# Kernel tuning notes

Measured on AMD Instinct MI355X. Metric: run time of the kernel, lower is better.

The kernel has to match this reference:

```python
import jax, jax.numpy as jnp
import numpy as np

N_NODES = 100000
N_EDGES = 3200000
N_FEAT = 300
HIDDEN = 32
N_CLASSES = 10


def setup_inputs() -> dict:
    key = jax.random.key(0)
    k1, k2, k3, k4 = jax.random.split(key, 4)
    x = jax.random.normal(k1, (N_NODES, N_FEAT), dtype=jnp.float32)
    edge_index = jax.random.randint(k2, (2, N_EDGES), 0, N_NODES, dtype=jnp.int64)
    # Glorot-ish init for weights
    W1 = jax.random.normal(k3, (N_FEAT, HIDDEN), dtype=jnp.float32) * (1.0 / np.sqrt(N_FEAT))
    b1 = jnp.zeros((HIDDEN,), dtype=jnp.float32)
    W2 = jax.random.normal(k4, (HIDDEN, N_CLASSES), dtype=jnp.float32) * (1.0 / np.sqrt(HIDDEN))
    b2 = jnp.zeros((N_CLASSES,), dtype=jnp.float32)
    return {"x": x, "edge_index": edge_index, "W1": W1, "b1": b1, "W2": W2, "b2": b2}


def reference(x, edge_index, W1, b1, W2, b2):
    N = x.shape[0]
    # GCNConv default: add self-loops, symmetric normalization deg^-1/2 A deg^-1/2
    loops = jnp.arange(N, dtype=edge_index.dtype)
    src = jnp.concatenate([edge_index[0], loops])  # message sources
    dst = jnp.concatenate([edge_index[1], loops])  # aggregation targets

    deg = jax.ops.segment_sum(jnp.ones(dst.shape, dtype=x.dtype), dst, num_segments=N)
    dinv = jnp.where(deg > 0, jax.lax.rsqrt(deg), 0.0)
    norm = dinv[src] * dinv[dst]  # [E+N]

    def gcn_conv(h, W, b):
        h = h @ W                                   # [N, out] dense GEMM first (linear-then-propagate)
        msg = h[src] * norm[:, None]                # gather + scale
        out = jax.ops.segment_sum(msg, dst, num_segments=N)  # scatter-add aggregate
        return out + b

    h = jnp.tanh(gcn_conv(x, W1, b1))
    # dropout p=0.5 is identity in eval mode (training=False)
    logits = gcn_conv(h, W2, b2)
    return jax.nn.log_softmax(logits, axis=1)
```

## Files before the change

### kernel.cpp

```cpp
#include <hip/hip_runtime.h>
#include <math.h>
#include <float.h>

#define NFEAT 300
#define HID 32
#define NCLS 10
#define GP 16
#define BSZ 128
#define TILE 8192

__global__ void k_zero_i(int* __restrict__ p, int n) {
    int i = blockIdx.x * 256 + threadIdx.x;
    if (i < n) p[i] = 0;
}

__global__ __launch_bounds__(256) void k_bhist(const int* __restrict__ ei, int E, int NB,
                                               int* __restrict__ bcnt) {
    __shared__ int h[1024];
    for (int i = threadIdx.x; i < NB; i += 256) h[i] = 0;
    __syncthreads();
    for (long long i = (long long)blockIdx.x * 256 + threadIdx.x; i < E;
         i += (long long)gridDim.x * 256)
        atomicAdd(&h[ei[E + i] >> 7], 1);
    __syncthreads();
    for (int i = threadIdx.x; i < NB; i += 256) {
        int v = h[i];
        if (v) atomicAdd(&bcnt[i], v);
    }
}

__global__ void k_bscan(const int* __restrict__ bcnt, int NB, int E,
                        int* __restrict__ bases, int* __restrict__ bcur) {
    __shared__ int s[1024];
    int tid = threadIdx.x;
    int v = (tid < NB) ? bcnt[tid] : 0;
    s[tid] = v;
    __syncthreads();
    for (int off = 1; off < 1024; off <<= 1) {
        int t = (tid >= off) ? s[tid - off] : 0;
        __syncthreads();
        s[tid] += t;
        __syncthreads();
    }
    if (tid < NB) {
        int ex = s[tid] - v;
        bases[tid] = ex;
        bcur[tid] = ex;
        if (tid == NB - 1) bases[NB] = E;
    }
}

__global__ __launch_bounds__(256) void k_part(const int* __restrict__ ei, int E, int NB,
                                              int* __restrict__ bcur, int* __restrict__ pp) {
    __shared__ int hist[1024], lbase[1024], gbase[1024], lcur[1024];
    __shared__ int stage[TILE], tgt[TILE];
    int* part = gbase;
    int tid = threadIdx.x;
    long long t0 = (long long)blockIdx.x * TILE;
    int nE = (int)(((long long)E - t0 < TILE) ? ((long long)E - t0) : TILE);

    for (int b = tid; b < NB; b += 256) hist[b] = 0;
    __syncthreads();
    for (int i = tid; i < nE; i += 256) {
        int d = ei[E + t0 + i];
        atomicAdd(&hist[d >> 7], 1);
    }
    __syncthreads();
    int i0 = tid * 4;
    int c0 = (i0 + 0 < NB) ? hist[i0 + 0] : 0;
    int c1 = (i0 + 1 < NB) ? hist[i0 + 1] : 0;
    int c2 = (i0 + 2 < NB) ? hist[i0 + 2] : 0;
    int c3 = (i0 + 3 < NB) ? hist[i0 + 3] : 0;
    int sum = c0 + c1 + c2 + c3;
    part[tid] = sum;
    __syncthreads();
    for (int off = 1; off < 256; off <<= 1) {
        int t = (tid >= off) ? part[tid - off] : 0;
        __syncthreads();
        part[tid] += t;
        __syncthreads();
    }
    int ex = part[tid] - sum;
    if (i0 + 0 < NB) { lbase[i0 + 0] = ex; ex += c0; }
    if (i0 + 1 < NB) { lbase[i0 + 1] = ex; ex += c1; }
    if (i0 + 2 < NB) { lbase[i0 + 2] = ex; ex += c2; }
    if (i0 + 3 < NB) { lbase[i0 + 3] = ex; ex += c3; }
    __syncthreads();
    for (int b = tid; b < NB; b += 256) {
        int h = hist[b];
        gbase[b] = h ? atomicAdd(&bcur[b], h) : 0;
        lcur[b] = 0;
    }
    __syncthreads();
    for (int i = tid; i < nE; i += 256) {
        int s = ei[t0 + i];
        int d = ei[E + t0 + i];
        int b = d >> 7;
        int lo = atomicAdd(&lcur[b], 1);
        int slot = lbase[b] + lo;
        stage[slot] = ((d - (b << 7)) << 17) | s;
        tgt[slot] = gbase[b] + lo;
    }
    __syncthreads();
    for (int i = tid; i < nE; i += 256)
        pp[tgt[i]] = stage[i];
}

__global__ __launch_bounds__(256) void k_csr(const int* __restrict__ pp,
                                             const int* __restrict__ bases,
                                             int N, int E,
                                             int* __restrict__ rowptr,
                                             float* __restrict__ dinv,
                                             int* __restrict__ col) {
    __shared__ int lc[BSZ], rp[BSZ], sc[BSZ];
    int b = blockIdx.x, tid = threadIdx.x;
    int n0 = b << 7;
    int base = bases[b];
    int cnt = bases[b + 1] - base;
    if (tid < BSZ) lc[tid] = 0;
    __syncthreads();
    for (int i = tid; i < cnt; i += 256)
        atomicAdd(&lc[pp[base + i] >> 17], 1);
    __syncthreads();
    if (tid < BSZ) sc[tid] = lc[tid];
    __syncthreads();
    for (int off = 1; off < BSZ; off <<= 1) {
        int t = (tid < BSZ && tid >= off) ? sc[tid - off] : 0;
        __syncthreads();
        if (tid < BSZ) sc[tid] += t;
        __syncthreads();
    }
    if (tid < BSZ) {
        int node = n0 + tid;
        int ex = base + sc[tid] - lc[tid];
        rp[tid] = ex;
        if (node < N) {
            rowptr[node] = ex;
            dinv[node] = rsqrtf((float)(lc[tid] + 1));
            if (node == N - 1) rowptr[N] = E;
        }
        lc[tid] = 0;
    }
    __syncthreads();
    for (int i = tid; i < cnt; i += 256) {
        int v = pp[base + i];
        int dl = v >> 17;
        int lo = atomicAdd(&lc[dl], 1);
        col[rp[dl] + lo] = v & 0x1FFFF;
    }
}

__global__ __launch_bounds__(256) void k_gemm1(const float* __restrict__ x,
                                               const float* __restrict__ W1,
                                               const float* __restrict__ dinv,
                                               float* __restrict__ h1s, int n) {
    int lane = threadIdx.x & 63;
    int q = __builtin_amdgcn_readfirstlane(threadIdx.x >> 6);
    int node = blockIdx.x * 64 + lane;
    bool valid = node < n;
    const float4* xr = reinterpret_cast<const float4*>(
        x + (size_t)(valid ? node : (n - 1)) * NFEAT);
    const float* Wq = W1 + q * 8;
    float acc[8];
#pragma unroll
    for (int i = 0; i < 8; ++i) acc[i] = 0.f;
#pragma unroll 5
    for (int c = 0; c < NFEAT / 4; ++c) {
        float4 xv = xr[c];
        const float* w0 = Wq + (size_t)(4 * c + 0) * HID;
        const float* w1 = Wq + (size_t)(4 * c + 1) * HID;
        const float* w2 = Wq + (size_t)(4 * c + 2) * HID;
        const float* w3 = Wq + (size_t)(4 * c + 3) * HID;
#pragma unroll
        for (int i = 0; i < 8; ++i) {
            acc[i] = fmaf(xv.x, w0[i], acc[i]);
            acc[i] = fmaf(xv.y, w1[i], acc[i]);
            acc[i] = fmaf(xv.z, w2[i], acc[i]);
            acc[i] = fmaf(xv.w, w3[i], acc[i]);
        }
    }
    if (valid) {
        float dd = dinv[node];
        float4* dst = reinterpret_cast<float4*>(h1s + (size_t)node * HID + q * 8);
        dst[0] = make_float4(dd * acc[0], dd * acc[1], dd * acc[2], dd * acc[3]);
        dst[1] = make_float4(dd * acc[4], dd * acc[5], dd * acc[6], dd * acc[7]);
    }
}

__global__ __launch_bounds__(256) void k_agg1(const float* __restrict__ h1s,
                                              const int* __restrict__ rowptr,
                                              const int* __restrict__ col,
                                              const float* __restrict__ dinv,
                                              const float* __restrict__ b1,
                                              float* __restrict__ h2, int n) {
    int node = blockIdx.x * 32 + (threadIdx.x >> 3);
    int l = threadIdx.x & 7;
    if (node >= n) return;
    const float4* h4 = reinterpret_cast<const float4*>(h1s);
    int beg = rowptr[node], end = rowptr[node + 1];
    float4 a0 = h4[(size_t)node * 8 + l];
    float4 a1 = make_float4(0.f, 0.f, 0.f, 0.f);
    float4 a2 = make_float4(0.f, 0.f, 0.f, 0.f);
    float4 a3 = make_float4(0.f, 0.f, 0.f, 0.f);
    int j = beg;
    for (; j + 3 < end; j += 4) {
        int s0 = col[j], s1 = col[j + 1], s2 = col[j + 2], s3 = col[j + 3];
        float4 v0 = h4[(size_t)s0 * 8 + l];
        float4 v1 = h4[(size_t)s1 * 8 + l];
        float4 v2 = h4[(size_t)s2 * 8 + l];
        float4 v3 = h4[(size_t)s3 * 8 + l];
        a0.x += v0.x; a0.y += v0.y; a0.z += v0.z; a0.w += v0.w;
        a1.x += v1.x; a1.y += v1.y; a1.z += v1.z; a1.w += v1.w;
        a2.x += v2.x; a2.y += v2.y; a2.z += v2.z; a2.w += v2.w;
        a3.x += v3.x; a3.y += v3.y; a3.z += v3.z; a3.w += v3.w;
    }
    for (; j < end; ++j) {
        float4 v = h4[(size_t)col[j] * 8 + l];
        a0.x += v.x; a0.y += v.y; a0.z += v.z; a0.w += v.w;
    }
    float dd = dinv[node];
    const float4* b4 = reinterpret_cast<const float4*>(b1);
    float4 bv = b4[l];
    float4 r;
    r.x = tanhf(fmaf(dd, (a0.x + a1.x) + (a2.x + a3.x), bv.x));
    r.y = tanhf(fmaf(dd, (a0.y + a1.y) + (a2.y + a3.y), bv.y));
    r.z = tanhf(fmaf(dd, (a0.z + a1.z) + (a2.z + a3.z), bv.z));
    r.w = tanhf(fmaf(dd, (a0.w + a1.w) + (a2.w + a3.w), bv.w));
    reinterpret_cast<float4*>(h2)[(size_t)node * 8 + l] = r;
}

__global__ __launch_bounds__(256) void k_gemm2(const float* __restrict__ h2,
                                               const float* __restrict__ W2,
                                               const float* __restrict__ dinv,
                                               float* __restrict__ gs, int n) {
    __shared__ float Ws[HID * NCLS];
    for (int i = threadIdx.x; i < HID * NCLS; i += 256) Ws[i] = W2[i];
    __syncthreads();
    int t = blockIdx.x * 256 + threadIdx.x;
    int node = t >> 4, c = t & 15;
    if (node >= n || c >= NCLS) return;
    const float* hr = h2 + (size_t)node * HID;
    float acc = 0.f;
#pragma unroll
    for (int k = 0; k < HID; ++k) acc = fmaf(hr[k], Ws[k * NCLS + c], acc);
    gs[(size_t)node * GP + c] = acc * dinv[node];
}

__global__ __launch_bounds__(256) void k_agg2(const float* __restrict__ gs,
                                              const int* __restrict__ rowptr,
                                              const int* __restrict__ col,
                                              const float* __restrict__ dinv,
                                              const float* __restrict__ b2,
                                              float* __restrict__ out, int n) {
    int node = blockIdx.x * 64 + (threadIdx.x >> 2);
    int l = threadIdx.x & 3;
    if (node >= n) return;
    const float4* g4 = reinterpret_cast<const float4*>(gs);
    int beg = rowptr[node], end = rowptr[node + 1];
    float4 a0 = g4[(size_t)node * 4 + l];
    float4 a1 = make_float4(0.f, 0.f, 0.f, 0.f);
    int j = beg;
    for (; j + 1 < end; j += 2) {
        int s0 = col[j], s1 = col[j + 1];
        float4 v0 = g4[(size_t)s0 * 4 + l];
        float4 v1 = g4[(size_t)s1 * 4 + l];
        a0.x += v0.x; a0.y += v0.y; a0.z += v0.z; a0.w += v0.w;
        a1.x += v1.x; a1.y += v1.y; a1.z += v1.z; a1.w += v1.w;
    }
    if (j < end) {
        float4 v = g4[(size_t)col[j] * 4 + l];
        a0.x += v.x; a0.y += v.y; a0.z += v.z; a0.w += v.w;
    }
    float dd = dinv[node];
    int c0 = 4 * l;
    float val[4];
    float av[4] = {a0.x + a1.x, a0.y + a1.y, a0.z + a1.z, a0.w + a1.w};
#pragma unroll
    for (int i = 0; i < 4; ++i) {
        int c = c0 + i;
        val[i] = (c < NCLS) ? fmaf(dd, av[i], b2[c]) : -FLT_MAX;
    }
    float m = fmaxf(fmaxf(val[0], val[1]), fmaxf(val[2], val[3]));
    m = fmaxf(m, __shfl_xor(m, 1, 4));
    m = fmaxf(m, __shfl_xor(m, 2, 4));
    float s = 0.f;
#pragma unroll
    for (int i = 0; i < 4; ++i)
        if (c0 + i < NCLS) s += expf(val[i] - m);
    s += __shfl_xor(s, 1, 4);
    s += __shfl_xor(s, 2, 4);
    float ls = m + logf(s);
    float* orow = out + (size_t)node * NCLS;
#pragma unroll
    for (int i = 0; i < 4; ++i)
        if (c0 + i < NCLS) orow[c0 + i] = val[i] - ls;
}

static inline size_t align256(size_t b) { return (b + 255) & ~(size_t)255; }

extern "C" void kernel_launch(void* const* d_in, const int* in_sizes, int n_in,
                              void* d_out, int out_size, void* d_ws, size_t ws_size,
                              hipStream_t stream) {
    const float* x  = (const float*)d_in[0];
    const int*   ei = (const int*)d_in[1];
    const float* W1 = (const float*)d_in[2];
    const float* b1 = (const float*)d_in[3];
    const float* W2 = (const float*)d_in[4];
    const float* b2 = (const float*)d_in[5];
    float* out = (float*)d_out;

    const int N = in_sizes[0] / NFEAT;
    const int E = in_sizes[1] / 2;
    const int NB = (N + BSZ - 1) / BSZ;

    char* p = (char*)d_ws;
    int* bcnt   = (int*)p;  p += align256(1024 * 4);
    int* bases  = (int*)p;  p += align256(1025 * 4);
    int* bcur   = (int*)p;  p += align256(1024 * 4);
    int* rowptr = (int*)p;  p += align256((size_t)(N + 1) * 4);
    int* pp     = (int*)p;  p += align256((size_t)E * 4);
    int* col    = (int*)p;  p += align256((size_t)E * 4);
    float* dinv = (float*)p; p += align256((size_t)N * 4);
    float* h1s  = (float*)p; p += align256((size_t)N * HID * 4);
    float* h2   = (float*)p; p += align256((size_t)N * HID * 4);
    float* gs   = h1s;

    dim3 B(256);
    int nT = (E + TILE - 1) / TILE;

    k_zero_i<<<4, B, 0, stream>>>(bcnt, 1024);
    k_bhist<<<128, B, 0, stream>>>(ei, E, NB, bcnt);
    k_bscan<<<1, 1024, 0, stream>>>(bcnt, NB, E, bases, bcur);
    k_part<<<nT, B, 0, stream>>>(ei, E, NB, bcur, pp);
    k_csr<<<NB, B, 0, stream>>>(pp, bases, N, E, rowptr, dinv, col);

    k_gemm1<<<(N + 63) / 64, B, 0, stream>>>(x, W1, dinv, h1s, N);
    k_agg1<<<(N + 31) / 32, B, 0, stream>>>(h1s, rowptr, col, dinv, b1, h2, N);
    k_gemm2<<<(N * 16 + 255) / 256, B, 0, stream>>>(h2, W2, dinv, gs, N);
    k_agg2<<<(N + 63) / 64, B, 0, stream>>>(gs, rowptr, col, dinv, b2, out, N);
}
```

Before: 260.0 us.

## Stage x rows through double-buffered LDS with coalesced loads in GEMM1

The first-layer GEMM previously had each lane stream its own 1200-byte x row with strided float4 loads, giving poorly coalesced global access. The kernel now cooperatively loads 64 rows in 60-feature chunks with coalesced float4 reads into padded shared memory (stride 61 to avoid bank conflicts), double-buffered so the next chunk's global loads are issued in registers before computing the current chunk. This adds LDS usage (about 31 KB per block) and block barriers, which may reduce occupancy.

```diff
diff --git a/kernel.cpp b/kernel.cpp
--- a/kernel.cpp
+++ b/kernel.cpp
@@ -154,32 +154,63 @@
                                                const float* __restrict__ W1,
                                                const float* __restrict__ dinv,
                                                float* __restrict__ h1s, int n) {
-    int lane = threadIdx.x & 63;
-    int q = __builtin_amdgcn_readfirstlane(threadIdx.x >> 6);
-    int node = blockIdx.x * 64 + lane;
-    bool valid = node < n;
-    const float4* xr = reinterpret_cast<const float4*>(
-        x + (size_t)(valid ? node : (n - 1)) * NFEAT);
-    const float* Wq = W1 + q * 8;
+    __shared__ float xs[2][64 * 61];
+    int tid = threadIdx.x;
+    int lane = tid & 63;
+    int q = __builtin_amdgcn_readfirstlane(tid >> 6);
+    int n0 = blockIdx.x * 64;
+    int node = n0 + lane;
+    const float4* x4 = reinterpret_cast<const float4*>(x);
+
     float acc[8];
 #pragma unroll
     for (int i = 0; i < 8; ++i) acc[i] = 0.f;
-#pragma unroll 5
-    for (int c = 0; c < NFEAT / 4; ++c) {
-        float4 xv = xr[c];
-        const float* w0 = Wq + (size_t)(4 * c + 0) * HID;
-        const float* w1 = Wq + (size_t)(4 * c + 1) * HID;
-        const float* w2 = Wq + (size_t)(4 * c + 2) * HID;
-        const float* w3 = Wq + (size_t)(4 * c + 3) * HID;
-#pragma unroll
-        for (int i = 0; i < 8; ++i) {
-            acc[i] = fmaf(xv.x, w0[i], acc[i]);
-            acc[i] = fmaf(xv.y, w1[i], acc[i]);
-            acc[i] = fmaf(xv.z, w2[i], acc[i]);
-            acc[i] = fmaf(xv.w, w3[i], acc[i]);
+
+    for (int i = tid; i < 960; i += 256) {
+        int r = i / 15, f = i % 15;
+        int gr = min(n0 + r, n - 1);
+        float4 v = x4[(size_t)gr * 75 + f];
+        float* d = &xs[0][r * 61 + f * 4];
+        d[0] = v.x; d[1] = v.y; d[2] = v.z; d[3] = v.w;
+    }
+    __syncthreads();
+
+    int cur = 0;
+    for (int ch = 0; ch < 5; ++ch) {
+        float4 v0, v1, v2, v3;
+        int i0 = tid, i1 = tid + 256, i2 = tid + 512, i3 = tid + 768;
+        bool more = (ch + 1 < 5);
+        if (more) {
+            int cb = (ch + 1) * 15;
+            { int r = i0 / 15, f = i0 % 15; v0 = x4[(size_t)min(n0 + r, n - 1) * 75 + cb + f]; }
+            { int r = i1 / 15, f = i1 % 15; v1 = x4[(size_t)min(n0 + r, n - 1) * 75 + cb + f]; }
+            { int r = i2 / 15, f = i2 % 15; v2 = x4[(size_t)min(n0 + r, n - 1) * 75 + cb + f]; }
+            if (i3 < 960) { int r = i3 / 15, f = i3 % 15; v3 = x4[(size_t)min(n0 + r, n - 1) * 75 + cb + f]; }
         }
-    }
-    if (valid) {
+        const float* xrow = &xs[cur][lane * 61];
+        const float* wbase = W1 + (size_t)(ch * 60) * HID + q * 8;
+#pragma unroll 6
+        for (int j = 0; j < 60; ++j) {
+            float xv = xrow[j];
+            const float* w = wbase + (size_t)j * HID;
+#pragma unroll
+            for (int i = 0; i < 8; ++i) acc[i] = fmaf(xv, w[i], acc[i]);
+        }
+        if (more) {
+            float* xb = xs[cur ^ 1];
+            { int r = i0 / 15, f = i0 % 15; float* d = &xb[r * 61 + f * 4];
+              d[0] = v0.x; d[1] = v0.y; d[2] = v0.z; d[3] = v0.w; }
+            { int r = i1 / 15, f = i1 % 15; float* d = &xb[r * 61 + f * 4];
+              d[0] = v1.x; d[1] = v1.y; d[2] = v1.z; d[3] = v1.w; }
+            { int r = i2 / 15, f = i2 % 15; float* d = &xb[r * 61 + f * 4];
+              d[0] = v2.x; d[1] = v2.y; d[2] = v2.z; d[3] = v2.w; }
+            if (i3 < 960) { int r = i3 / 15, f = i3 % 15; float* d = &xb[r * 61 + f * 4];
+              d[0] = v3.x; d[1] = v3.y; d[2] = v3.z; d[3] = v3.w; }
+        }
+        __syncthreads();
+        cur ^= 1;
+    }
+    if (node < n) {
         float dd = dinv[node];
         float4* dst = reinterpret_cast<float4*>(h1s + (size_t)node * HID + q * 8);
         dst[0] = make_float4(dd * acc[0], dd * acc[1], dd * acc[2], dd * acc[3]);
```

Result: no change. 261.7 us (median of 5 runs) (+0.7%).

## Stage x and W1 chunks through shared memory in first GEMM

Applied to the files above, without the earlier changes.

Rewrites the x@W1 kernel to cooperatively load 128-node by 48-feature tiles of x, plus the matching W1 rows, into shared memory. Each thread then computes 16 outputs instead of 8, so the x row is read once per block rather than by four waves. The old version had each lane stream its own 1200-byte x row with strided float4 loads. The new one coalesces global reads across the block and reuses W through LDS float4 broadcasts, at the cost of block syncs and more registers.

```diff
diff --git a/kernel.cpp b/kernel.cpp
--- a/kernel.cpp
+++ b/kernel.cpp
@@ -154,36 +154,64 @@
                                                const float* __restrict__ W1,
                                                const float* __restrict__ dinv,
                                                float* __restrict__ h1s, int n) {
-    int lane = threadIdx.x & 63;
-    int q = __builtin_amdgcn_readfirstlane(threadIdx.x >> 6);
-    int node = blockIdx.x * 64 + lane;
-    bool valid = node < n;
-    const float4* xr = reinterpret_cast<const float4*>(
-        x + (size_t)(valid ? node : (n - 1)) * NFEAT);
-    const float* Wq = W1 + q * 8;
-    float acc[8];
-#pragma unroll
-    for (int i = 0; i < 8; ++i) acc[i] = 0.f;
-#pragma unroll 5
-    for (int c = 0; c < NFEAT / 4; ++c) {
-        float4 xv = xr[c];
-        const float* w0 = Wq + (size_t)(4 * c + 0) * HID;
-        const float* w1 = Wq + (size_t)(4 * c + 1) * HID;
-        const float* w2 = Wq + (size_t)(4 * c + 2) * HID;
-        const float* w3 = Wq + (size_t)(4 * c + 3) * HID;
-#pragma unroll
-        for (int i = 0; i < 8; ++i) {
-            acc[i] = fmaf(xv.x, w0[i], acc[i]);
-            acc[i] = fmaf(xv.y, w1[i], acc[i]);
-            acc[i] = fmaf(xv.z, w2[i], acc[i]);
-            acc[i] = fmaf(xv.w, w3[i], acc[i]);
+    __shared__ float xs[128 * 49];
+    __shared__ float Wc[48 * HID];
+    int tid = threadIdx.x;
+    int lane = tid & 63;
+    int w = __builtin_amdgcn_readfirstlane(tid >> 6);
+    int g = w & 1;
+    int p = w >> 1;
+    int n0 = blockIdx.x * 128;
+    int node = n0 + 64 * g + lane;
+    const float4* x4 = reinterpret_cast<const float4*>(x);
+    const float4* w4 = reinterpret_cast<const float4*>(W1);
+
+    float acc[16];
+#pragma unroll
+    for (int i = 0; i < 16; ++i) acc[i] = 0.f;
+
+    for (int ch = 0; ch < 7; ++ch) {
+        int j0 = ch * 48;
+        int CL = (NFEAT - j0 < 48) ? (NFEAT - j0) : 48;
+        int nf4 = CL >> 2;
+        __syncthreads();
+        int tot = 128 * nf4;
+        for (int i = tid; i < tot; i += 256) {
+            int r = i / nf4, f = i - r * nf4;
+            int gr = min(n0 + r, n - 1);
+            float4 v = x4[(size_t)gr * 75 + ch * 12 + f];
+            float* d = &xs[r * 49 + f * 4];
+            d[0] = v.x; d[1] = v.y; d[2] = v.z; d[3] = v.w;
         }
-    }
-    if (valid) {
+        for (int i = tid; i < CL * 8; i += 256)
+            reinterpret_cast<float4*>(Wc)[i] = w4[(size_t)j0 * 8 + i];
+        __syncthreads();
+        const float* xrow = &xs[(64 * g + lane) * 49];
+        const float4* Wq = reinterpret_cast<const float4*>(Wc) + 4 * p;
+#pragma unroll 4
+        for (int j = 0; j < CL; ++j) {
+            float xv = xrow[j];
+            float4 w0 = Wq[j * 8 + 0];
+            float4 w1 = Wq[j * 8 + 1];
+            float4 w2 = Wq[j * 8 + 2];
+            float4 w3 = Wq[j * 8 + 3];
+            acc[0]  = fmaf(xv, w0.x, acc[0]);  acc[1]  = fmaf(xv, w0.y, acc[1]);
+            acc[2]  = fmaf(xv, w0.z, acc[2]);  acc[3]  = fmaf(xv, w0.w, acc[3]);
+            acc[4]  = fmaf(xv, w1.x, acc[4]);  acc[5]  = fmaf(xv, w1.y, acc[5]);
+            acc[6]  = fmaf(xv, w1.z, acc[6]);  acc[7]  = fmaf(xv, w1.w, acc[7]);
+            acc[8]  = fmaf(xv, w2.x, acc[8]);  acc[9]  = fmaf(xv, w2.y, acc[9]);
+            acc[10] = fmaf(xv, w2.z, acc[10]); acc[11] = fmaf(xv, w2.w, acc[11]);
+            acc[12] = fmaf(xv, w3.x, acc[12]); acc[13] = fmaf(xv, w3.y, acc[13]);
+            acc[14] = fmaf(xv, w3.z, acc[14]); acc[15] = fmaf(xv, w3.w, acc[15]);
+        }
+    }
+    if (node < n) {
         float dd = dinv[node];
-        float4* dst = reinterpret_cast<float4*>(h1s + (size_t)node * HID + q * 8);
-        dst[0] = make_float4(dd * acc[0], dd * acc[1], dd * acc[2], dd * acc[3]);
-        dst[1] = make_float4(dd * acc[4], dd * acc[5], dd * acc[6], dd * acc[7]);
+        float4* dst = reinterpret_cast<float4*>(h1s + (size_t)node * HID + 16 * p);
+#pragma unroll
+        for (int qq = 0; qq < 4; ++qq)
+            dst[qq] = make_float4(dd * acc[4 * qq], dd * acc[4 * qq + 1],
+                                  dd * acc[4 * qq + 2], dd * acc[4 * qq + 3]);
     }
 }
 
@@ -334,7 +362,7 @@
     k_part<<<nT, B, 0, stream>>>(ei, E, NB, bcur, pp);
     k_csr<<<NB, B, 0, stream>>>(pp, bases, N, E, rowptr, dinv, col);
 
-    k_gemm1<<<(N + 63) / 64, B, 0, stream>>>(x, W1, dinv, h1s, N);
+    k_gemm1<<<(N + 127) / 128, B, 0, stream>>>(x, W1, dinv, h1s, N);
     k_agg1<<<(N + 31) / 32, B, 0, stream>>>(h1s, rowptr, col, dinv, b1, h2, N);
     k_gemm2<<<(N * 16 + 255) / 256, B, 0, stream>>>(h2, W2, dinv, gs, N);
     k_agg2<<<(N + 63) / 64, B, 0, stream>>>(gs, rowptr, col, dinv, b2, out, N);
```

Result: slower. 276.6 us (+6.4%).

## Tile first-layer GEMM through double-buffered shared memory with register blocking

Applied to the files above, without the earlier changes.

Rewrites the x·W1 kernel so each 256-thread block handles 256 nodes. Feature chunks of x and W1 are staged through double-buffered LDS, using coalesced float4 global loads prefetched into registers, and each thread computes a 4-node × 8-output tile. This replaces the old per-thread strided row reads and repeated global W loads, aiming to make the 120 MB x stream coalesced and bandwidth-bound. In exchange it uses larger LDS and register footprints, launches about four times fewer blocks, and reads dinv as a float4 past N in the last block.

```diff
diff --git a/kernel.cpp b/kernel.cpp
--- a/kernel.cpp
+++ b/kernel.cpp
@@ -8,6 +8,7 @@
 #define GP 16
 #define BSZ 128
 #define TILE 8192
+#define XS 264
 
 __global__ void k_zero_i(int* __restrict__ p, int n) {
     int i = blockIdx.x * 256 + threadIdx.x;
@@ -154,36 +155,97 @@
                                                const float* __restrict__ W1,
                                                const float* __restrict__ dinv,
                                                float* __restrict__ h1s, int n) {
-    int lane = threadIdx.x & 63;
-    int q = __builtin_amdgcn_readfirstlane(threadIdx.x >> 6);
-    int node = blockIdx.x * 64 + lane;
-    bool valid = node < n;
-    const float4* xr = reinterpret_cast<const float4*>(
-        x + (size_t)(valid ? node : (n - 1)) * NFEAT);
-    const float* Wq = W1 + q * 8;
-    float acc[8];
-#pragma unroll
-    for (int i = 0; i < 8; ++i) acc[i] = 0.f;
-#pragma unroll 5
-    for (int c = 0; c < NFEAT / 4; ++c) {
-        float4 xv = xr[c];
-        const float* w0 = Wq + (size_t)(4 * c + 0) * HID;
-        const float* w1 = Wq + (size_t)(4 * c + 1) * HID;
-        const float* w2 = Wq + (size_t)(4 * c + 2) * HID;
-        const float* w3 = Wq + (size_t)(4 * c + 3) * HID;
-#pragma unroll
-        for (int i = 0; i < 8; ++i) {
-            acc[i] = fmaf(xv.x, w0[i], acc[i]);
-            acc[i] = fmaf(xv.y, w1[i], acc[i]);
-            acc[i] = fmaf(xv.z, w2[i], acc[i]);
-            acc[i] = fmaf(xv.w, w3[i], acc[i]);
+    __shared__ float xs[2][24 * XS];
+    __shared__ float Wc[2][24 * HID];
+    const int tid = threadIdx.x;
+    const int lane = tid & 63;
+    const int w = __builtin_amdgcn_readfirstlane(tid >> 6);
+    const int n0 = blockIdx.x * 256;
+    const float4* x4 = reinterpret_cast<const float4*>(x);
+    const float4* w4 = reinterpret_cast<const float4*>(W1);
+
+    float acc[32];
+#pragma unroll
+    for (int i = 0; i < 32; ++i) acc[i] = 0.f;
+
+    float4 u[6];
+    float4 wreg;
+#pragma unroll
+    for (int m = 0; m < 6; ++m) {
+        int idx = m * 256 + tid, r = idx / 6, fq = idx % 6;
+        u[m] = x4[(size_t)min(n0 + r, n - 1) * 75 + fq];
+    }
+    if (tid < 192) wreg = w4[tid];
+
+    int cur = 0;
+    for (int ch = 0; ch < 13; ++ch) {
+        const int CL = (ch == 12) ? 12 : 24;
+        if (CL == 24) {
+#pragma unroll
+            for (int m = 0; m < 6; ++m) {
+                int idx = m * 256 + tid, r = idx / 6, fq = idx % 6;
+                float* d = &xs[cur][(fq * 4) * XS + r];
+                d[0] = u[m].x; d[XS] = u[m].y; d[2 * XS] = u[m].z; d[3 * XS] = u[m].w;
+            }
+            if (tid < 192) reinterpret_cast<float4*>(Wc[cur])[tid] = wreg;
+        } else {
+#pragma unroll
+            for (int m = 0; m < 3; ++m) {
+                int idx = m * 256 + tid, r = idx / 3, fq = idx % 3;
+                float* d = &xs[cur][(fq * 4) * XS + r];
+                d[0] = u[m].x; d[XS] = u[m].y; d[2 * XS] = u[m].z; d[3 * XS] = u[m].w;
+            }
+            if (tid < 96) reinterpret_cast<float4*>(Wc[cur])[tid] = wreg;
         }
-    }
-    if (valid) {
-        float dd = dinv[node];
-        float4* dst = reinterpret_cast<float4*>(h1s + (size_t)node * HID + q * 8);
-        dst[0] = make_float4(dd * acc[0], dd * acc[1], dd * acc[2], dd * acc[3]);
-        dst[1] = make_float4(dd * acc[4], dd * acc[5], dd * acc[6], dd * acc[7]);
+        __syncthreads();
+        if (ch < 12) {
+            int nch = ch + 1;
+            if (nch < 12) {
+#pragma unroll
+                for (int m = 0; m < 6; ++m) {
+                    int idx = m * 256 + tid, r = idx / 6, fq = idx % 6;
+                    u[m] = x4[(size_t)min(n0 + r, n - 1) * 75 + nch * 6 + fq];
+                }
+                if (tid < 192) wreg = w4[nch * 192 + tid];
+            } else {
+#pragma unroll
+                for (int m = 0; m < 3; ++m) {
+                    int idx = m * 256 + tid, r = idx / 3, fq = idx % 3;
+                    u[m] = x4[(size_t)min(n0 + r, n - 1) * 75 + 72 + fq];
+                }
+                if (tid < 96) wreg = w4[12 * 192 + tid];
+            }
+        }
+        const float* xr = &xs[cur][4 * lane];
+        const float* wr = &Wc[cur][8 * w];
+#pragma unroll 4
+        for (int j = 0; j < CL; ++j) {
+            float4 xv = *reinterpret_cast<const float4*>(xr + j * XS);
+            float4 w0 = *reinterpret_cast<const float4*>(wr + j * HID);
+            float4 w1 = *reinterpret_cast<const float4*>(wr + j * HID + 4);
+            float xn[4] = {xv.x, xv.y, xv.z, xv.w};
+            float wk[8] = {w0.x, w0.y, w0.z, w0.w, w1.x, w1.y, w1.z, w1.w};
+#pragma unroll
+            for (int nn = 0; nn < 4; ++nn)
+#pragma unroll
+                for (int kk = 0; kk < 8; ++kk)
+                    acc[nn * 8 + kk] = fmaf(xn[nn], wk[kk], acc[nn * 8 + kk]);
+        }
+        cur ^= 1;
+    }
+    float4 dv = reinterpret_cast<const float4*>(dinv + n0)[lane];
+    float dvv[4] = {dv.x, dv.y, dv.z, dv.w};
+#pragma unroll
+    for (int nn = 0; nn < 4; ++nn) {
+        int node = n0 + 4 * lane + nn;
+        if (node < n) {
+            float dd = dvv[nn];
+            float4* dst = reinterpret_cast<float4*>(h1s + (size_t)node * HID + 8 * w);
+            dst[0] = make_float4(dd * acc[nn * 8 + 0], dd * acc[nn * 8 + 1],
+                                 dd * acc[nn * 8 + 2], dd * acc[nn * 8 + 3]);
+            dst[1] = make_float4(dd * acc[nn * 8 + 4], dd * acc[nn * 8 + 5],
+                                 dd * acc[nn * 8 + 6], dd * acc[nn * 8 + 7]);
+        }
     }
 }
 
@@ -334,7 +396,7 @@
     k_part<<<nT, B, 0, stream>>>(ei, E, NB, bcur, pp);
     k_csr<<<NB, B, 0, stream>>>(pp, bases, N, E, rowptr, dinv, col);
 
-    k_gemm1<<<(N + 63) / 64, B, 0, stream>>>(x, W1, dinv, h1s, N);
+    k_gemm1<<<(N + 255) / 256, B, 0, stream>>>(x, W1, dinv, h1s, N);
     k_agg1<<<(N + 31) / 32, B, 0, stream>>>(h1s, rowptr, col, dinv, b1, h2, N);
     k_gemm2<<<(N * 16 + 255) / 256, B, 0, stream>>>(h2, W2, dinv, gs, N);
     k_agg2<<<(N + 63) / 64, B, 0, stream>>>(gs, rowptr, col, dinv, b2, out, N);
```

After: 264.2 us. About the same (+1.6%).
